# Optimization experiments

Measured on AMD Instinct MI355X. Metric: run time of the kernel, lower is better.

The kernel has to match this reference:

```python
import jax, jax.numpy as jnp
import numpy as np

N_NODES = 50000
N_EDGES = 1000000
IN_CH = 128
OUT_CH = 128
N_HEADS = 8
CIS = 8.0


def _edge_conv(x, e, wq, bq, wk, bk, wv, bv, n_heads, cis):
    """One EdgeConv layer (PyG mean aggregation, source_to_target flow)."""
    src, dst = e[0], e[1]                       # x_j = x[src], x_i = x[dst]
    xi = x[dst]
    xj = x[src]
    feat = jnp.concatenate([xi, xj - xi], axis=1)        # [E, 2C]
    q = feat @ wq + bq                                   # [E, O]
    k = feat @ wk + bk
    v = feat @ wv + bv
    E, O = q.shape
    hs = O // n_heads
    q = q.reshape(E, n_heads, hs)
    k = k.reshape(E, n_heads, hs)
    v = v.reshape(E, n_heads, hs)
    # edge_weight = sign(log|dst-src| - log(cis))
    d = jnp.abs(dst - src).astype(q.dtype)
    ew = jnp.sign(jnp.log(d) - jnp.log(jnp.asarray(cis, q.dtype)))
    v = v * ew[:, None, None]
    scale = jnp.asarray(1.0 / np.sqrt(hs), q.dtype)
    probs = jax.nn.softmax(q * k * scale, axis=-1)       # softmax over head_size
    ctx = (probs * v).reshape(E, O)                      # [E, O]
    n = x.shape[0]
    s = jax.ops.segment_sum(ctx, dst, num_segments=n)    # mean aggr over targets
    cnt = jax.ops.segment_sum(jnp.ones((E,), ctx.dtype), dst, num_segments=n)
    return s / jnp.maximum(cnt, 1.0)[:, None]


def setup_inputs() -> dict:
    key = jax.random.key(0)
    ks = jax.random.split(key, 24)
    x = jax.random.normal(ks[0], (N_NODES, IN_CH), jnp.float32)
    edge_index = jax.random.randint(ks[1], (2, N_EDGES), 0, N_NODES, dtype=jnp.int32)
    half = N_EDGES // 2
    e0 = edge_index[:, jax.random.permutation(ks[2], N_EDGES)[:half]]
    e1 = edge_index[:, jax.random.permutation(ks[3], N_EDGES)[:half]]
    e2 = edge_index[:, jax.random.permutation(ks[4], N_EDGES)[:half]]
    batch = jnp.zeros((N_NODES,), jnp.int32)

    def mk(k, i, o):
        return jax.random.normal(k, (i, o), jnp.float32) * 0.02

    def mkb(k, o):
        return jax.random.normal(k, (o,), jnp.float32) * 0.02

    # layer dims: conv0 128->128, conv1 128->64, conv2 64->128
    return dict(
        x=x, e0=e0, e1=e1, e2=e2, batch=batch,
        wq0=mk(ks[5], 2 * IN_CH, OUT_CH), bq0=mkb(ks[6], OUT_CH),
        wk0=mk(ks[7], 2 * IN_CH, OUT_CH), bk0=mkb(ks[8], OUT_CH),
        wv0=mk(ks[9], 2 * IN_CH, OUT_CH), bv0=mkb(ks[10], OUT_CH),
        wq1=mk(ks[11], 2 * OUT_CH, OUT_CH // 2), bq1=mkb(ks[12], OUT_CH // 2),
        wk1=mk(ks[13], 2 * OUT_CH, OUT_CH // 2), bk1=mkb(ks[14], OUT_CH // 2),
        wv1=mk(ks[15], 2 * OUT_CH, OUT_CH // 2), bv1=mkb(ks[16], OUT_CH // 2),
        wq2=mk(ks[17], OUT_CH, OUT_CH), bq2=mkb(ks[18], OUT_CH),
        wk2=mk(ks[19], OUT_CH, OUT_CH), bk2=mkb(ks[20], OUT_CH),
        wv2=mk(ks[21], OUT_CH, OUT_CH), bv2=mkb(ks[22], OUT_CH),
    )


def reference(x, e0, e1, e2, batch,
              wq0, bq0, wk0, bk0, wv0, bv0,
              wq1, bq1, wk1, bk1, wv1, bv1,
              wq2, bq2, wk2, bk2, wv2, bv2):
    x0 = jax.nn.relu(_edge_conv(x, e0, wq0, bq0, wk0, bk0, wv0, bv0, N_HEADS, CIS))
    h = jax.nn.relu(_edge_conv(x0, e1, wq1, bq1, wk1, bk1, wv1, bv1, N_HEADS, CIS))
    h = _edge_conv(h, e2, wq2, bq2, wk2, bk2, wv2, bv2, N_HEADS, CIS)
    return jax.nn.relu(h + x0)
```

## Files before the change

kernel.cpp:

```cpp
#include <hip/hip_runtime.h>


typedef short bf16x8 __attribute__((ext_vector_type(8)));
typedef float f32x4 __attribute__((ext_vector_type(4)));

__device__ __forceinline__ unsigned short f2bf(float f) {
  unsigned int u = __float_as_uint(f);
  u += 0x7FFFu + ((u >> 16) & 1u);
  return (unsigned short)(u >> 16);
}
__device__ __forceinline__ float b2f(short s) {
  return __uint_as_float(((unsigned)(unsigned short)s) << 16);
}

__device__ __forceinline__ void pack_w_seg(const float* __restrict__ wq,
                                           const float* __restrict__ wk,
                                           const float* __restrict__ wv,
                                           unsigned short* __restrict__ dst,
                                           int IN, int O, float kscale, int id) {
  int kchunks = IN >> 5, nchunks = O >> 4;
  int total = 6 * nchunks * kchunks * 64;
  if (id >= total) return;
  int lane = id & 63;
  int frag = id >> 6;
  int kc = frag % kchunks;
  int nc = (frag / kchunks) % nchunks;
  int mat = frag / (kchunks * nchunks);
  const float* w = (mat % 3 == 0) ? wq : (mat % 3 == 1) ? wk : wv;
  float mul = (mat % 3 == 1) ? kscale : 1.0f;
  int n = nc * 16 + (lane & 15);
  int k0 = kc * 32 + (lane >> 4) * 8;
  unsigned short tmp[8];
#pragma unroll
  for (int j = 0; j < 8; ++j) {
    int row = k0 + j;
    float bot = w[(size_t)(IN + row) * O + n];
    float val = (mat < 3) ? (w[(size_t)row * O + n] - bot) : bot;
    tmp[j] = f2bf(val * mul);
  }
  uint4 o;
  o.x = (unsigned)tmp[0] | ((unsigned)tmp[1] << 16);
  o.y = (unsigned)tmp[2] | ((unsigned)tmp[3] << 16);
  o.z = (unsigned)tmp[4] | ((unsigned)tmp[5] << 16);
  o.w = (unsigned)tmp[6] | ((unsigned)tmp[7] << 16);
  reinterpret_cast<uint4*>(dst)[id] = o;
}

__global__ void pack_weights_fused(
    const float* __restrict__ wq0, const float* __restrict__ wk0, const float* __restrict__ wv0,
    const float* __restrict__ wq1, const float* __restrict__ wk1, const float* __restrict__ wv1,
    const float* __restrict__ wq2, const float* __restrict__ wk2, const float* __restrict__ wv2,
    unsigned short* __restrict__ wp0, unsigned short* __restrict__ wp1,
    unsigned short* __restrict__ wp2, float sc16, float sc8) {
  int id = blockIdx.x * blockDim.x + threadIdx.x;
  if (blockIdx.x < 48) {
    pack_w_seg(wq0, wk0, wv0, wp0, 128, 128, sc16, id);
  } else if (blockIdx.x < 72) {
    pack_w_seg(wq1, wk1, wv1, wp1, 128, 64, sc8, id - 48 * 256);
  } else {
    pack_w_seg(wq2, wk2, wv2, wp2, 64, 128, sc16, id - 72 * 256);
  }
}

__device__ __forceinline__ void pack_b_seg(const float* __restrict__ bq,
                                           const float* __restrict__ bk,
                                           const float* __restrict__ bv, float kscale, int O,
                                           float* __restrict__ out, int i) {
  int mat = i / O, c = i % O;
  float v = 0.f;
  if (mat == 0) v = bq[c];
  else if (mat == 1) v = bk[c] * kscale;
  else if (mat == 2) v = bv[c];
  out[i] = v;
}

__global__ void pack_bias_fused(
    const float* __restrict__ bq0, const float* __restrict__ bk0, const float* __restrict__ bv0,
    const float* __restrict__ bq1, const float* __restrict__ bk1, const float* __restrict__ bv1,
    const float* __restrict__ bq2, const float* __restrict__ bk2, const float* __restrict__ bv2,
    float* __restrict__ bias0, float* __restrict__ bias1, float* __restrict__ bias2,
    float sc16, float sc8) {
  int i = blockIdx.x * blockDim.x + threadIdx.x;
  if (i < 768) pack_b_seg(bq0, bk0, bv0, sc16, 128, bias0, i);
  else if (i < 1152) pack_b_seg(bq1, bk1, bv1, sc8, 64, bias1, i - 768);
  else if (i < 1920) pack_b_seg(bq2, bk2, bv2, sc16, 128, bias2, i - 1152);
}

__global__ void zero3(uint4* __restrict__ a, int na, uint4* __restrict__ b, int nb,
                      uint4* __restrict__ c, int nc) {
  const uint4 z = make_uint4(0u, 0u, 0u, 0u);
  const int stride = gridDim.x * blockDim.x;
  const int t0 = blockIdx.x * blockDim.x + threadIdx.x;
  for (int j = t0; j < na; j += stride) a[j] = z;
  for (int j = t0; j < nb; j += stride) b[j] = z;
  for (int j = t0; j < nc; j += stride) c[j] = z;
}

__global__ void hist3(const int* __restrict__ e0, const int* __restrict__ e1,
                      const int* __restrict__ e2, int E, int* __restrict__ hist,
                      int* __restrict__ rank, int NP) {
  int i = blockIdx.x * blockDim.x + threadIdx.x;
  if (i >= E) return;
  rank[0 * E + i] = atomicAdd(&hist[0 * NP + e0[E + i]], 1);
  rank[1 * E + i] = atomicAdd(&hist[1 * NP + e1[E + i]], 1);
  rank[2 * E + i] = atomicAdd(&hist[2 * NP + e2[E + i]], 1);
}

__device__ __forceinline__ int block_scan_excl256(int v, int* buf, int t, int* total) {
  buf[t] = v;
  __syncthreads();
#pragma unroll
  for (int off = 1; off < 256; off <<= 1) {
    int add = (t >= off) ? buf[t - off] : 0;
    __syncthreads();
    buf[t] += add;
    __syncthreads();
  }
  int incl = buf[t];
  *total = buf[255];
  __syncthreads();
  return incl - v;
}

__global__ void scan_pass1(const int* __restrict__ hist, int* __restrict__ excl,
                           int* __restrict__ bsum, int n, int NP) {
  __shared__ int buf[256];
  int y = blockIdx.y, t = threadIdx.x;
  int i = blockIdx.x * 256 + t;
  int v = (i < n) ? hist[y * NP + i] : 0;
  int total;
  int ex = block_scan_excl256(v, buf, t, &total);
  if (i < NP) excl[y * NP + i] = ex;
  if (t == 0) bsum[y * 256 + blockIdx.x] = total;
}

__global__ void scan_pass2(int* __restrict__ bsum, int nblk) {
  __shared__ int buf[256];
  int y = blockIdx.y, t = threadIdx.x;
  int v = (t < nblk) ? bsum[y * 256 + t] : 0;
  int total;
  int ex = block_scan_excl256(v, buf, t, &total);
  bsum[y * 256 + t] = ex;
}

__global__ void scan_pass3(const int* __restrict__ excl, const int* __restrict__ bsum,
                           int* __restrict__ rowptr, int n, int NP, int RP, int E) {
  int y = blockIdx.y;
  int i = blockIdx.x * 256 + threadIdx.x;
  if (i < n) rowptr[y * RP + i] = excl[y * NP + i] + bsum[y * 256 + blockIdx.x];
  if (i == 0) rowptr[y * RP + n] = E;
}

__global__ void scatter3(const int* __restrict__ e0, const int* __restrict__ e1,
                         const int* __restrict__ e2, int E, const int* __restrict__ rowptr,
                         const int* __restrict__ rank, long long* __restrict__ pairs,
                         int NP, int RP) {
  int y = blockIdx.y;
  const int* e = (y == 0) ? e0 : (y == 1) ? e1 : e2;
  int i = blockIdx.x * 256 + threadIdx.x;
  if (i >= E) return;
  int sN = e[i], d = e[E + i];
  int pos = rowptr[y * RP + d] + rank[(size_t)y * E + i];
  long long val = ((long long)(unsigned)d << 32) | (unsigned)sN;
  __builtin_nontemporal_store(val, &pairs[(size_t)y * E + pos]);
}

template <int IN, int O, int G>
__global__ __launch_bounds__(256, 4) void node_gemm(
    const unsigned short* __restrict__ xb, int N, int NT,
    const unsigned short* __restrict__ wpack, const float* __restrict__ bias6,
    unsigned short* __restrict__ Y1, unsigned short* __restrict__ Y2) {
  constexpr int KC = IN / 32;
  constexpr int NCH = O / 16;
  constexpr int CHR = IN / 8;
  constexpr int CM = CHR - 1;
  __shared__ unsigned short tiles[64 * IN];

  const int chunk = gridDim.x >> 3;
  const int lb = (blockIdx.x & 7) * chunk + (blockIdx.x >> 3);
  if (lb >= NT * G) return;
  const int tile = lb / G;
  const int grp = lb % G;

  const int t = threadIdx.x, w = t >> 6, ln = t & 63;
  const int n0 = tile * 64;

  {
    constexpr int RPI = 64 / CHR;
    constexpr int NI = 16 / RPI;
    const int r_in = ln / CHR, c = ln % CHR;
#pragma unroll
    for (int i = 0; i < NI; ++i) {
      int row = w * 16 + i * RPI + r_in;
      int node = min(n0 + row, N - 1);
      int sc = c ^ (row & CM);
      const unsigned short* g = xb + (size_t)node * IN + sc * 8;
      unsigned short* l = &tiles[(size_t)(w * 16 + i * RPI) * IN];
      __builtin_amdgcn_global_load_lds(
          (const __attribute__((address_space(1))) unsigned int*)g,
          (__attribute__((address_space(3))) unsigned int*)l, 16, 0, 0);
    }
  }
  __syncthreads();

  const int col = ln & 15, quad = ln >> 4;
  const int g0 = grp * 8 + w * 2;

  f32x4 acc[2][4];
#pragma unroll
  for (int cc = 0; cc < 2; ++cc)
#pragma unroll
    for (int m = 0; m < 4; ++m) acc[cc][m] = (f32x4){0.f, 0.f, 0.f, 0.f};

#pragma unroll
  for (int kc = 0; kc < KC; ++kc) {
    bf16x8 a[4];
#pragma unroll
    for (int m = 0; m < 4; ++m) {
      int row = m * 16 + col;
      int sc = (kc * 4 + quad) ^ (row & CM);
      a[m] = *reinterpret_cast<const bf16x8*>(&tiles[(size_t)row * IN + sc * 8]);
    }
#pragma unroll
    for (int cc = 0; cc < 2; ++cc) {
      const bf16x8 b = *reinterpret_cast<const bf16x8*>(
          wpack + ((size_t)((g0 + cc) * KC + kc) * 64 + ln) * 8);
#pragma unroll
      for (int m = 0; m < 4; ++m)
        acc[cc][m] = __builtin_amdgcn_mfma_f32_16x16x32_bf16(a[m], b, acc[cc][m], 0, 0, 0);
    }
  }

#pragma unroll
  for (int cc = 0; cc < 2; ++cc) {
    int gch = g0 + cc;
    int mat = gch / NCH, ncg = gch % NCH;
    unsigned short* Yp = (mat < 3) ? Y1 : Y2;
    int mo = (mat < 3) ? mat : mat - 3;
    float bv = bias6[gch * 16 + col];
    size_t coloff = (size_t)mo * O + ncg * 16 + col;
#pragma unroll
    for (int m = 0; m < 4; ++m)
#pragma unroll
      for (int r = 0; r < 4; ++r) {
        int node = n0 + m * 16 + quad * 4 + r;
        if (node < N) Yp[(size_t)node * (3 * O) + coloff] = f2bf(acc[cc][m][r] + bv);
      }
  }
}

template <int O, int HS>
__global__ __launch_bounds__(512, 6) void edge_attn_kernel(
    const unsigned short* __restrict__ Y1, const unsigned short* __restrict__ Y2,
    const int2* __restrict__ pairs, const int E, float* __restrict__ s) {
  constexpr int NL = HS / 8;
  constexpr int PM = O / 4 - 1;
  __shared__ float ctx[64 * O];
  __shared__ int dstL[64];

  const int chunkB = gridDim.x >> 3;
  const int lb = (blockIdx.x & 7) * chunkB + (blockIdx.x >> 3);
  if (lb * 64 >= E) return;

  const int t = threadIdx.x;
  const int e = t >> 3, head = t & 7;
  const int eG = lb * 64 + e;
  const int eC = min(eG, E - 1);
  const bool valid = eG < E;
  const int2 p = pairs[eC];
  const int sN = p.x, dN = p.y;
  if ((t & 7) == 0) dstL[e] = dN;
  const float dd = fabsf((float)(dN - sN));
  const float ew = (dd > 8.f) ? 1.f : ((dd == 8.f) ? 0.f : -1.f);

  const unsigned short* b1 = Y1 + (size_t)dN * (3 * O) + head * HS;
  const unsigned short* b2 = Y2 + (size_t)sN * (3 * O) + head * HS;

  bf16x8 q1[NL], q2[NL], k1[NL], k2[NL], v1[NL], v2[NL];
#pragma unroll
  for (int l = 0; l < NL; ++l) {
    q1[l] = *reinterpret_cast<const bf16x8*>(b1 + l * 8);
    q2[l] = *reinterpret_cast<const bf16x8*>(b2 + l * 8);
    k1[l] = *reinterpret_cast<const bf16x8*>(b1 + O + l * 8);
    k2[l] = *reinterpret_cast<const bf16x8*>(b2 + O + l * 8);
    v1[l] = *reinterpret_cast<const bf16x8*>(b1 + 2 * O + l * 8);
    v2[l] = *reinterpret_cast<const bf16x8*>(b2 + 2 * O + l * 8);
  }

  float ex[HS];
  float sum = 0.f;
#pragma unroll
  for (int l = 0; l < NL; ++l)
#pragma unroll
    for (int j = 0; j < 8; ++j) {
      float q = b2f(q1[l][j]) + b2f(q2[l][j]);
      float k = b2f(k1[l][j]) + b2f(k2[l][j]);
      float eo = __expf(q * k);
      ex[l * 8 + j] = eo;
      sum += eo;
    }
  const float rs = valid ? (ew / sum) : 0.f;
#pragma unroll
  for (int l = 0; l < NL; ++l) {
#pragma unroll
    for (int g2 = 0; g2 < 2; ++g2) {
      f32x4 o;
#pragma unroll
      for (int j2 = 0; j2 < 4; ++j2) {
        int j = g2 * 4 + j2;
        o[j2] = ex[l * 8 + j] * rs * (b2f(v1[l][j]) + b2f(v2[l][j]));
      }
      int g = l * 2 + g2;
      int pch = (g * 8 + head + e) & PM;
      *reinterpret_cast<f32x4*>(&ctx[e * O + pch * 4]) = o;
    }
  }
  __syncthreads();

  {
    constexpr int GRP = 512 / O;
    constexpr int EPT = 64 / GRP;
    const int hs2 = t & 7;
    const int cs = (t >> 3) & (HS - 1);
    const int colA = hs2 * HS + cs;
    const int seg0 = (t / O) * EPT;
    const int inv = (cs >> 2) * 8 + hs2;
    const int js = cs & 3;
    float run = 0.f;
#pragma unroll
    for (int i = 0; i < EPT; ++i) {
      int ee = seg0 + i;
      int pch = (inv + ee) & PM;
      run += ctx[ee * O + pch * 4 + js];
      bool bound = (i == EPT - 1) || (dstL[ee + 1] != dstL[ee]);
      if (bound) {
        atomicAdd(&s[(size_t)dstL[ee] * O + colA], run);
        run = 0.f;
      }
    }
  }
}

__global__ void f32_to_bf16(const float* __restrict__ in, unsigned short* __restrict__ out,
                            int n8) {
  int i = blockIdx.x * blockDim.x + threadIdx.x;
  if (i >= n8) return;
  float4 a = reinterpret_cast<const float4*>(in)[2 * i];
  float4 b = reinterpret_cast<const float4*>(in)[2 * i + 1];
  uint4 o;
  o.x = (unsigned)f2bf(a.x) | ((unsigned)f2bf(a.y) << 16);
  o.y = (unsigned)f2bf(a.z) | ((unsigned)f2bf(a.w) << 16);
  o.z = (unsigned)f2bf(b.x) | ((unsigned)f2bf(b.y) << 16);
  o.w = (unsigned)f2bf(b.z) | ((unsigned)f2bf(b.w) << 16);
  reinterpret_cast<uint4*>(out)[i] = o;
}

__global__ void finalize_relu_f32bf16(float* __restrict__ s, const int* __restrict__ rowptr,
                                      unsigned short* __restrict__ xbo, int total4, int Odiv4) {
  int i = blockIdx.x * blockDim.x + threadIdx.x;
  if (i >= total4) return;
  int node = i / Odiv4;
  float c = fmaxf((float)(rowptr[node + 1] - rowptr[node]), 1.0f);
  float4 v = reinterpret_cast<float4*>(s)[i];
  v.x = fmaxf(v.x / c, 0.f);
  v.y = fmaxf(v.y / c, 0.f);
  v.z = fmaxf(v.z / c, 0.f);
  v.w = fmaxf(v.w / c, 0.f);
  reinterpret_cast<float4*>(s)[i] = v;
  ushort4 o = make_ushort4(f2bf(v.x), f2bf(v.y), f2bf(v.z), f2bf(v.w));
  reinterpret_cast<ushort4*>(xbo)[i] = o;
}

__global__ void finalize_relu_bf16(const float* __restrict__ s, const int* __restrict__ rowptr,
                                   unsigned short* __restrict__ xbo, int total4, int Odiv4) {
  int i = blockIdx.x * blockDim.x + threadIdx.x;
  if (i >= total4) return;
  int node = i / Odiv4;
  float c = fmaxf((float)(rowptr[node + 1] - rowptr[node]), 1.0f);
  float4 v = reinterpret_cast<const float4*>(s)[i];
  ushort4 o = make_ushort4(f2bf(fmaxf(v.x / c, 0.f)), f2bf(fmaxf(v.y / c, 0.f)),
                           f2bf(fmaxf(v.z / c, 0.f)), f2bf(fmaxf(v.w / c, 0.f)));
  reinterpret_cast<ushort4*>(xbo)[i] = o;
}

__global__ void finalize_add_relu(float* __restrict__ out, const float* __restrict__ x0,
                                  const int* __restrict__ rowptr, int total4, int Odiv4) {
  int i = blockIdx.x * blockDim.x + threadIdx.x;
  if (i >= total4) return;
  int node = i / Odiv4;
  float c = fmaxf((float)(rowptr[node + 1] - rowptr[node]), 1.0f);
  float4 v = reinterpret_cast<float4*>(out)[i];
  float4 r = reinterpret_cast<const float4*>(x0)[i];
  v.x = fmaxf(v.x / c + r.x, 0.f);
  v.y = fmaxf(v.y / c + r.y, 0.f);
  v.z = fmaxf(v.z / c + r.z, 0.f);
  v.w = fmaxf(v.w / c + r.w, 0.f);
  reinterpret_cast<float4*>(out)[i] = v;
}

extern "C" void kernel_launch(void* const* d_in, const int* in_sizes, int n_in,
                              void* d_out, int out_size, void* d_ws, size_t ws_size,
                              hipStream_t stream) {
  const float* x = (const float*)d_in[0];
  const int* e0 = (const int*)d_in[1];
  const int* e1 = (const int*)d_in[2];
  const int* e2 = (const int*)d_in[3];
  const float* wq0 = (const float*)d_in[5];
  const float* bq0 = (const float*)d_in[6];
  const float* wk0 = (const float*)d_in[7];
  const float* bk0 = (const float*)d_in[8];
  const float* wv0 = (const float*)d_in[9];
  const float* bv0 = (const float*)d_in[10];
  const float* wq1 = (const float*)d_in[11];
  const float* bq1 = (const float*)d_in[12];
  const float* wk1 = (const float*)d_in[13];
  const float* bk1 = (const float*)d_in[14];
  const float* wv1 = (const float*)d_in[15];
  const float* bv1 = (const float*)d_in[16];
  const float* wq2 = (const float*)d_in[17];
  const float* bq2 = (const float*)d_in[18];
  const float* wk2 = (const float*)d_in[19];
  const float* bk2 = (const float*)d_in[20];
  const float* wv2 = (const float*)d_in[21];
  const float* bv2 = (const float*)d_in[22];

  const int N = in_sizes[0] / 128;
  const int E = in_sizes[1] / 2;
  const int NBLK = (N + 255) / 256;
  const int NP = NBLK * 256;
  const int RP = NP + 256;
  const float SC16 = 0.25f;
  const float SC8 = 0.35355339059327373f;

  unsigned short* wp0 = (unsigned short*)d_ws;
  unsigned short* wp1 = wp0 + 98304;
  unsigned short* wp2 = wp1 + 49152;
  float* bias0 = (float*)(wp2 + 49152);
  float* bias1 = bias0 + 768;
  float* bias2 = bias1 + 384;
  unsigned short* xb = (unsigned short*)(bias2 + 768);
  unsigned short* Y1 = xb + (size_t)N * 128;
  unsigned short* Y2 = Y1 + (size_t)N * 384;
  float* s0 = (float*)(Y2 + (size_t)N * 384);
  float* s1 = s0 + (size_t)N * 128;
  int* hist = (int*)(s1 + (size_t)N * 64);
  int* excl = hist + 3 * (size_t)NP;
  int* bsum = excl + 3 * (size_t)NP;
  int* rowptr = bsum + 768;
  int* rank = rowptr + 3 * (size_t)RP;
  long long* pairs = (long long*)(rank + 3 * (size_t)E + 2);

  zero3<<<2048, 256, 0, stream>>>((uint4*)hist, 3 * NP / 4, (uint4*)s0, N * 48,
                                  (uint4*)d_out, out_size / 4);

  pack_weights_fused<<<96, 256, 0, stream>>>(wq0, wk0, wv0, wq1, wk1, wv1, wq2, wk2, wv2,
                                             wp0, wp1, wp2, SC16, SC8);
  pack_bias_fused<<<8, 256, 0, stream>>>(bq0, bk0, bv0, bq1, bk1, bv1, bq2, bk2, bv2,
                                         bias0, bias1, bias2, SC16, SC8);
  f32_to_bf16<<<(N * 16 + 255) / 256, 256, 0, stream>>>(x, xb, N * 16);

  const int EB256 = (E + 255) / 256;
  hist3<<<EB256, 256, 0, stream>>>(e0, e1, e2, E, hist, rank, NP);
  scan_pass1<<<dim3(NBLK, 3), 256, 0, stream>>>(hist, excl, bsum, N, NP);
  scan_pass2<<<dim3(1, 3), 256, 0, stream>>>(bsum, NBLK);
  scan_pass3<<<dim3(NBLK, 3), 256, 0, stream>>>(excl, bsum, rowptr, N, NP, RP, E);
  scatter3<<<dim3(EB256, 3), 256, 0, stream>>>(e0, e1, e2, E, rowptr, rank, pairs, NP, RP);

  const int NT = (N + 63) / 64;
  const int EBK = (E + 63) / 64;
  const int EGRID = 8 * ((EBK + 7) / 8);
  const int GG6 = 8 * ((NT * 6 + 7) / 8);
  const int GG3 = 8 * ((NT * 3 + 7) / 8);

  node_gemm<128, 128, 6><<<GG6, 256, 0, stream>>>(xb, N, NT, wp0, bias0, Y1, Y2);
  edge_attn_kernel<128, 16><<<EGRID, 512, 0, stream>>>(Y1, Y2, (const int2*)pairs, E, s0);
  finalize_relu_f32bf16<<<(N * 32 + 255) / 256, 256, 0, stream>>>(s0, rowptr, xb, N * 32, 32);
  node_gemm<128, 64, 3><<<GG3, 256, 0, stream>>>(xb, N, NT, wp1, bias1, Y1, Y2);
  edge_attn_kernel<64, 8><<<EGRID, 512, 0, stream>>>(Y1, Y2, (const int2*)(pairs + E), E, s1);
  finalize_relu_bf16<<<(N * 16 + 255) / 256, 256, 0, stream>>>(s1, rowptr + RP, xb, N * 16, 16);
  node_gemm<64, 128, 6><<<GG6, 256, 0, stream>>>(xb, N, NT, wp2, bias2, Y1, Y2);
  edge_attn_kernel<128, 16><<<EGRID, 512, 0, stream>>>(Y1, Y2, (const int2*)(pairs + 2 * (size_t)E),
                                                       E, (float*)d_out);
  finalize_add_relu<<<(N * 32 + 255) / 256, 256, 0, stream>>>((float*)d_out, s0, rowptr + 2 * RP,
                                                              N * 32, 32);
}
```

Before: 554.8 us.

## Fuse preprocessing kernels, use exp2 with folded log2e, packed bf16 math, fewer atomics

Merges the zeroing, weight packing, bias packing and x-to-bf16 conversion kernels into one preproc launch to cut launch overhead. The attention kernel now folds log2(e) into the key scale so it can call exp2f, and unpacks bf16 pairs into float2 vectors to allow packed FP32 math. The segmented reduction writes interior runs (destinations fully contained in a thread's chunk) with plain stores instead of atomics, keeping atomics only for runs at chunk boundaries. The plain stores assume no other block contributes to those rows, which relies on the edges being sorted by destination.

```diff
diff --git a/kernel.cpp b/kernel.cpp
--- a/kernel.cpp
+++ b/kernel.cpp
@@ -2,7 +2,9 @@
 
 
 typedef short bf16x8 __attribute__((ext_vector_type(8)));
+typedef unsigned int u32x4 __attribute__((ext_vector_type(4)));
 typedef float f32x4 __attribute__((ext_vector_type(4)));
+typedef float f32x2 __attribute__((ext_vector_type(2)));
 
 __device__ __forceinline__ unsigned short f2bf(float f) {
   unsigned int u = __float_as_uint(f);
@@ -11,6 +13,12 @@
 }
 __device__ __forceinline__ float b2f(short s) {
   return __uint_as_float(((unsigned)(unsigned short)s) << 16);
+}
+__device__ __forceinline__ f32x2 bfpair(unsigned w) {
+  f32x2 r;
+  r.x = __uint_as_float(w << 16);
+  r.y = __uint_as_float(w & 0xffff0000u);
+  return r;
 }
 
 __device__ __forceinline__ void pack_w_seg(const float* __restrict__ wq,
@@ -46,22 +54,6 @@
   reinterpret_cast<uint4*>(dst)[id] = o;
 }
 
-__global__ void pack_weights_fused(
-    const float* __restrict__ wq0, const float* __restrict__ wk0, const float* __restrict__ wv0,
-    const float* __restrict__ wq1, const float* __restrict__ wk1, const float* __restrict__ wv1,
-    const float* __restrict__ wq2, const float* __restrict__ wk2, const float* __restrict__ wv2,
-    unsigned short* __restrict__ wp0, unsigned short* __restrict__ wp1,
-    unsigned short* __restrict__ wp2, float sc16, float sc8) {
-  int id = blockIdx.x * blockDim.x + threadIdx.x;
-  if (blockIdx.x < 48) {
-    pack_w_seg(wq0, wk0, wv0, wp0, 128, 128, sc16, id);
-  } else if (blockIdx.x < 72) {
-    pack_w_seg(wq1, wk1, wv1, wp1, 128, 64, sc8, id - 48 * 256);
-  } else {
-    pack_w_seg(wq2, wk2, wv2, wp2, 64, 128, sc16, id - 72 * 256);
-  }
-}
-
 __device__ __forceinline__ void pack_b_seg(const float* __restrict__ bq,
                                            const float* __restrict__ bk,
                                            const float* __restrict__ bv, float kscale, int O,
@@ -74,26 +66,45 @@
   out[i] = v;
 }
 
-__global__ void pack_bias_fused(
+__global__ void preproc(
+    uint4* __restrict__ z0, int n0, uint4* __restrict__ z1, int n1,
+    uint4* __restrict__ z2, int n2,
+    const float* __restrict__ x, unsigned short* __restrict__ xb, int n8,
+    const float* __restrict__ wq0, const float* __restrict__ wk0, const float* __restrict__ wv0,
+    const float* __restrict__ wq1, const float* __restrict__ wk1, const float* __restrict__ wv1,
+    const float* __restrict__ wq2, const float* __restrict__ wk2, const float* __restrict__ wv2,
+    unsigned short* __restrict__ wp0, unsigned short* __restrict__ wp1,
+    unsigned short* __restrict__ wp2,
     const float* __restrict__ bq0, const float* __restrict__ bk0, const float* __restrict__ bv0,
     const float* __restrict__ bq1, const float* __restrict__ bk1, const float* __restrict__ bv1,
     const float* __restrict__ bq2, const float* __restrict__ bk2, const float* __restrict__ bv2,
     float* __restrict__ bias0, float* __restrict__ bias1, float* __restrict__ bias2,
     float sc16, float sc8) {
-  int i = blockIdx.x * blockDim.x + threadIdx.x;
-  if (i < 768) pack_b_seg(bq0, bk0, bv0, sc16, 128, bias0, i);
-  else if (i < 1152) pack_b_seg(bq1, bk1, bv1, sc8, 64, bias1, i - 768);
-  else if (i < 1920) pack_b_seg(bq2, bk2, bv2, sc16, 128, bias2, i - 1152);
-}
-
-__global__ void zero3(uint4* __restrict__ a, int na, uint4* __restrict__ b, int nb,
-                      uint4* __restrict__ c, int nc) {
-  const uint4 z = make_uint4(0u, 0u, 0u, 0u);
+  const int tid = blockIdx.x * blockDim.x + threadIdx.x;
   const int stride = gridDim.x * blockDim.x;
-  const int t0 = blockIdx.x * blockDim.x + threadIdx.x;
-  for (int j = t0; j < na; j += stride) a[j] = z;
-  for (int j = t0; j < nb; j += stride) b[j] = z;
-  for (int j = t0; j < nc; j += stride) c[j] = z;
+  const uint4 Z = make_uint4(0u, 0u, 0u, 0u);
+  for (int j = tid; j < n0; j += stride) z0[j] = Z;
+  for (int j = tid; j < n1; j += stride) z1[j] = Z;
+  for (int j = tid; j < n2; j += stride) z2[j] = Z;
+  for (int j = tid; j < n8; j += stride) {
+    float4 a = reinterpret_cast<const float4*>(x)[2 * j];
+    float4 b = reinterpret_cast<const float4*>(x)[2 * j + 1];
+    uint4 o;
+    o.x = (unsigned)f2bf(a.x) | ((unsigned)f2bf(a.y) << 16);
+    o.y = (unsigned)f2bf(a.z) | ((unsigned)f2bf(a.w) << 16);
+    o.z = (unsigned)f2bf(b.x) | ((unsigned)f2bf(b.y) << 16);
+    o.w = (unsigned)f2bf(b.z) | ((unsigned)f2bf(b.w) << 16);
+    reinterpret_cast<uint4*>(xb)[j] = o;
+  }
+  if (tid < 12288) pack_w_seg(wq0, wk0, wv0, wp0, 128, 128, sc16, tid);
+  else if (tid < 18432) pack_w_seg(wq1, wk1, wv1, wp1, 128, 64, sc8, tid - 12288);
+  else if (tid < 24576) pack_w_seg(wq2, wk2, wv2, wp2, 64, 128, sc16, tid - 18432);
+  else if (tid < 24576 + 1920) {
+    int i = tid - 24576;
+    if (i < 768) pack_b_seg(bq0, bk0, bv0, sc16, 128, bias0, i);
+    else if (i < 1152) pack_b_seg(bq1, bk1, bv1, sc8, 64, bias1, i - 768);
+    else pack_b_seg(bq2, bk2, bv2, sc16, 128, bias2, i - 1152);
+  }
 }
 
 __global__ void hist3(const int* __restrict__ e0, const int* __restrict__ e1,
@@ -276,40 +287,43 @@
   const unsigned short* b1 = Y1 + (size_t)dN * (3 * O) + head * HS;
   const unsigned short* b2 = Y2 + (size_t)sN * (3 * O) + head * HS;
 
-  bf16x8 q1[NL], q2[NL], k1[NL], k2[NL], v1[NL], v2[NL];
+  u32x4 q1[NL], q2[NL], k1[NL], k2[NL], v1[NL], v2[NL];
 #pragma unroll
   for (int l = 0; l < NL; ++l) {
-    q1[l] = *reinterpret_cast<const bf16x8*>(b1 + l * 8);
-    q2[l] = *reinterpret_cast<const bf16x8*>(b2 + l * 8);
-    k1[l] = *reinterpret_cast<const bf16x8*>(b1 + O + l * 8);
-    k2[l] = *reinterpret_cast<const bf16x8*>(b2 + O + l * 8);
-    v1[l] = *reinterpret_cast<const bf16x8*>(b1 + 2 * O + l * 8);
-    v2[l] = *reinterpret_cast<const bf16x8*>(b2 + 2 * O + l * 8);
-  }
-
-  float ex[HS];
-  float sum = 0.f;
+    q1[l] = *reinterpret_cast<const u32x4*>(b1 + l * 8);
+    q2[l] = *reinterpret_cast<const u32x4*>(b2 + l * 8);
+    k1[l] = *reinterpret_cast<const u32x4*>(b1 + O + l * 8);
+    k2[l] = *reinterpret_cast<const u32x4*>(b2 + O + l * 8);
+    v1[l] = *reinterpret_cast<const u32x4*>(b1 + 2 * O + l * 8);
+    v2[l] = *reinterpret_cast<const u32x4*>(b2 + 2 * O + l * 8);
+  }
+
+  f32x2 ex2[NL * 4];
+  f32x2 sum2 = (f32x2){0.f, 0.f};
 #pragma unroll
   for (int l = 0; l < NL; ++l)
 #pragma unroll
-    for (int j = 0; j < 8; ++j) {
-      float q = b2f(q1[l][j]) + b2f(q2[l][j]);
-      float k = b2f(k1[l][j]) + b2f(k2[l][j]);
-      float eo = __expf(q * k);
-      ex[l * 8 + j] = eo;
-      sum += eo;
-    }
+    for (int d = 0; d < 4; ++d) {
+      f32x2 q = bfpair(q1[l][d]) + bfpair(q2[l][d]);
+      f32x2 k = bfpair(k1[l][d]) + bfpair(k2[l][d]);
+      f32x2 qk = q * k;
+      f32x2 eo;
+      eo.x = exp2f(qk.x);
+      eo.y = exp2f(qk.y);
+      ex2[l * 4 + d] = eo;
+      sum2 += eo;
+    }
+  const float sum = sum2.x + sum2.y;
   const float rs = valid ? (ew / sum) : 0.f;
+  const f32x2 rs2 = (f32x2){rs, rs};
 #pragma unroll
   for (int l = 0; l < NL; ++l) {
 #pragma unroll
     for (int g2 = 0; g2 < 2; ++g2) {
-      f32x4 o;
-#pragma unroll
-      for (int j2 = 0; j2 < 4; ++j2) {
-        int j = g2 * 4 + j2;
-        o[j2] = ex[l * 8 + j] * rs * (b2f(v1[l][j]) + b2f(v2[l][j]));
-      }
+      f32x2 oa = ex2[l * 4 + g2 * 2] * rs2 * (bfpair(v1[l][g2 * 2]) + bfpair(v2[l][g2 * 2]));
+      f32x2 ob = ex2[l * 4 + g2 * 2 + 1] * rs2 *
+                 (bfpair(v1[l][g2 * 2 + 1]) + bfpair(v2[l][g2 * 2 + 1]));
+      f32x4 o = (f32x4){oa.x, oa.y, ob.x, ob.y};
       int g = l * 2 + g2;
       int pch = (g * 8 + head + e) & PM;
       *reinterpret_cast<f32x4*>(&ctx[e * O + pch * 4]) = o;
@@ -327,32 +341,24 @@
     const int inv = (cs >> 2) * 8 + hs2;
     const int js = cs & 3;
     float run = 0.f;
+    int runstart = 0;
+    int dcur = dstL[seg0];
 #pragma unroll
     for (int i = 0; i < EPT; ++i) {
       int ee = seg0 + i;
       int pch = (inv + ee) & PM;
       run += ctx[ee * O + pch * 4 + js];
-      bool bound = (i == EPT - 1) || (dstL[ee + 1] != dstL[ee]);
-      if (bound) {
-        atomicAdd(&s[(size_t)dstL[ee] * O + colA], run);
+      int dnext = (i < EPT - 1) ? dstL[ee + 1] : -1;
+      if (dnext != dcur) {
+        float* addr = &s[(size_t)dcur * O + colA];
+        if (runstart > 0 && i < EPT - 1) *addr = run;
+        else atomicAdd(addr, run);
         run = 0.f;
+        runstart = i + 1;
+        dcur = dnext;
       }
     }
   }
-}
-
-__global__ void f32_to_bf16(const float* __restrict__ in, unsigned short* __restrict__ out,
-                            int n8) {
-  int i = blockIdx.x * blockDim.x + threadIdx.x;
-  if (i >= n8) return;
-  float4 a = reinterpret_cast<const float4*>(in)[2 * i];
-  float4 b = reinterpret_cast<const float4*>(in)[2 * i + 1];
-  uint4 o;
-  o.x = (unsigned)f2bf(a.x) | ((unsigned)f2bf(a.y) << 16);
-  o.y = (unsigned)f2bf(a.z) | ((unsigned)f2bf(a.w) << 16);
-  o.z = (unsigned)f2bf(b.x) | ((unsigned)f2bf(b.y) << 16);
-  o.w = (unsigned)f2bf(b.z) | ((unsigned)f2bf(b.w) << 16);
-  reinterpret_cast<uint4*>(out)[i] = o;
 }
 
 __global__ void finalize_relu_f32bf16(float* __restrict__ s, const int* __restrict__ rowptr,
@@ -429,8 +435,9 @@
   const int NBLK = (N + 255) / 256;
   const int NP = NBLK * 256;
   const int RP = NP + 256;
-  const float SC16 = 0.25f;
-  const float SC8 = 0.35355339059327373f;
+  const float LOG2E = 1.4426950408889634f;
+  const float SC16 = 0.25f * LOG2E;
+  const float SC8 = 0.35355339059327373f * LOG2E;
 
   unsigned short* wp0 = (unsigned short*)d_ws;
   unsigned short* wp1 = wp0 + 98304;
@@ -450,14 +457,12 @@
   int* rank = rowptr + 3 * (size_t)RP;
   long long* pairs = (long long*)(rank + 3 * (size_t)E + 2);
 
-  zero3<<<2048, 256, 0, stream>>>((uint4*)hist, 3 * NP / 4, (uint4*)s0, N * 48,
-                                  (uint4*)d_out, out_size / 4);
-
-  pack_weights_fused<<<96, 256, 0, stream>>>(wq0, wk0, wv0, wq1, wk1, wv1, wq2, wk2, wv2,
-                                             wp0, wp1, wp2, SC16, SC8);
-  pack_bias_fused<<<8, 256, 0, stream>>>(bq0, bk0, bv0, bq1, bk1, bv1, bq2, bk2, bv2,
-                                         bias0, bias1, bias2, SC16, SC8);
-  f32_to_bf16<<<(N * 16 + 255) / 256, 256, 0, stream>>>(x, xb, N * 16);
+  preproc<<<2048, 256, 0, stream>>>(
+      (uint4*)hist, 3 * NP / 4, (uint4*)s0, N * 48, (uint4*)d_out, out_size / 4,
+      x, xb, N * 16,
+      wq0, wk0, wv0, wq1, wk1, wv1, wq2, wk2, wv2, wp0, wp1, wp2,
+      bq0, bk0, bv0, bq1, bk1, bv1, bq2, bk2, bv2, bias0, bias1, bias2,
+      SC16, SC8);
 
   const int EB256 = (E + 255) / 256;
   hist3<<<EB256, 256, 0, stream>>>(e0, e1, e2, E, hist, rank, NP);
```

New measurement: 531.7 us. 4.2% less time.
